# Kernel tuning notes

Measured on AMD Instinct MI355X. Metric: run time of the kernel, lower is better.

The kernel has to match this reference:

```python
import jax, jax.numpy as jnp
import numpy as np

B, N, FD = 2, 50000, 13
E = 250000
M, H = 128, 128          # message_dim, hidden_dim
EDGE_IN = 2 * FD + 8     # 34
NODE_IN = FD + 2 * M     # 269


def _mlp(x, w1, b1, w2, b2):
    return jnp.tanh(x @ w1 + b1) @ w2 + b2


def setup_inputs() -> dict:
    root = jax.random.key(0)
    k = lambda i: jax.random.fold_in(root, i)

    def lin(i, din, dout):
        w = jax.random.normal(k(i), (din, dout), jnp.float32) * np.float32(1.0 / np.sqrt(din))
        b = jax.random.normal(k(i + 100), (dout,), jnp.float32) * np.float32(0.01)
        return w, b

    ew1, eb1 = lin(1, EDGE_IN, H); ew2, eb2 = lin(2, H, M)      # mlp_edge
    ww1, wb1 = lin(3, EDGE_IN, H); ww2, wb2 = lin(4, H, 1)      # mlp_weight
    xw1, xb1 = lin(5, EDGE_IN, H); xw2, xb2 = lin(6, H, M)      # mlp_edge_world
    yw1, yb1 = lin(7, EDGE_IN, H); yw2, yb2 = lin(8, H, 1)      # mlp_weight_world
    nw1, nb1 = lin(9, NODE_IN, H); nw2, nb2 = lin(10, H, FD)    # mlp_node

    z_h = jax.random.normal(k(20), (B, N, FD), jnp.float32)
    edge_hh = jax.random.randint(k(21), (B, 2, E), 0, N, jnp.int32)
    edge_world = jax.random.randint(k(22), (B, 2, E), 0, N, jnp.int32)
    return dict(z_h=z_h, edge_hh=edge_hh, edge_world=edge_world,
                ew1=ew1, eb1=eb1, ew2=ew2, eb2=eb2,
                ww1=ww1, wb1=wb1, ww2=ww2, wb2=wb2,
                xw1=xw1, xb1=xb1, xw2=xw2, xb2=xb2,
                yw1=yw1, yb1=yb1, yw2=yw2, yb2=yb2,
                nw1=nw1, nb1=nb1, nw2=nw2, nb2=nb2)


def _edge_features(z, s, t):
    # z: (N, FD); s, t: (E,)
    pos, vel = z[:, 0:3], z[:, 3:6]
    diff = pos[s] - pos[t]                               # (E, 3)
    dist = jnp.sum(diff * diff, axis=-1, keepdims=True)  # (E, 1) squared distance
    vxc = jnp.cross(vel[s], vel[t])                      # (E, 3)
    vxn = jnp.linalg.norm(vxc, axis=-1, keepdims=True)   # (E, 1)
    return jnp.concatenate([diff, dist, vxc, vxn], axis=-1)  # (E, 8)


def reference(z_h, edge_hh, edge_world,
              ew1, eb1, ew2, eb2, ww1, wb1, ww2, wb2,
              xw1, xb1, xw2, xb2, yw1, yb1, yw2, yb2,
              nw1, nb1, nw2, nb2):
    n_nodes = z_h.shape[1]

    def per_batch(z, e_hh, e_w):
        # normal edges
        s, t = e_hh[0], e_hh[1]
        inp = jnp.concatenate([z[s], z[t], _edge_features(z, s, t)], axis=-1)  # (E, 34)
        m = _mlp(inp, ew1, eb1, ew2, eb2)                                       # (E, M)
        w = jax.nn.sigmoid(_mlp(inp, ww1, wb1, ww2, wb2))                       # (E, 1)
        agg_h = jnp.zeros((n_nodes, M), z.dtype).at[t].add(w * m)
        # world edges
        sw, tw = e_w[0], e_w[1]
        inpw = jnp.concatenate([z[sw], z[tw], _edge_features(z, sw, tw)], axis=-1)
        mw = _mlp(inpw, xw1, xb1, xw2, xb2)
        ww_ = jax.nn.sigmoid(_mlp(inpw, yw1, yb1, yw2, yb2))
        agg_w = jnp.zeros((n_nodes, M), z.dtype).at[tw].add(ww_ * mw)
        return agg_h, agg_w

    m_agg_h, m_agg_w = jax.vmap(per_batch)(z_h, edge_hh, edge_world)  # (B, N, M) each
    input_node = jnp.concatenate([z_h, m_agg_h, m_agg_w], axis=-1)    # (B, N, 269)
    delta_z_h = _mlp(input_node, nw1, nb1, nw2, nb2)                  # (B, N, 13)
    return delta_z_h
```

## Files before the change

### kernel.cpp

```cpp
#include <hip/hip_runtime.h>
#include <hip/hip_bf16.h>

#define B_   2
#define N_   50000
#define FD_  13
#define E_   250000
#define M_   128
#define H_   128

typedef __attribute__((ext_vector_type(8))) short  short8;
typedef __attribute__((ext_vector_type(8))) __bf16 bf16x8;
typedef __attribute__((ext_vector_type(4))) float  f32x4;
typedef __attribute__((ext_vector_type(4))) unsigned int uint4v;
typedef __attribute__((ext_vector_type(8))) unsigned short ushort8;

#define AGG_BYTES  (4ull * N_ * 128 * 4)
#define HIST_BYTES (4ull * N_ * 4)
#define SORT_BYTES (4ull * E_ * 4)
#define OFF_EW1 0u
#define OFF_WW1 8192u
#define OFF_EW2 16384u
#define OFF_XW1 32768u
#define OFF_YW1 40960u
#define OFF_XW2 49152u
#define OFF_NW1 65536u
#define OFF_NW2 102400u

__device__ __forceinline__ float bf2f(unsigned short u) {
    unsigned int v = ((unsigned int)u) << 16;
    return __builtin_bit_cast(float, v);
}
__device__ __forceinline__ unsigned short f2bf(float f) {
    __bf16 h = (__bf16)f;
    return __builtin_bit_cast(unsigned short, h);
}
__device__ __forceinline__ float tanh_fast(float x) {
    float e = __expf(x + x);
    float r = __builtin_amdgcn_rcpf(e + 1.0f);
    return __builtin_fmaf(-2.0f, r, 1.0f);
}
__device__ __forceinline__ float sigmoid_fast(float x) {
    return __builtin_amdgcn_rcpf(1.0f + __expf(-x));
}
__device__ __forceinline__ f32x4 mfma16(short8 a, short8 b, f32x4 c) {
    return __builtin_amdgcn_mfma_f32_16x16x32_bf16(
        __builtin_bit_cast(bf16x8, a), __builtin_bit_cast(bf16x8, b), c, 0, 0, 0);
}

__global__ void prep_kernel(const float* __restrict__ ew1, const float* __restrict__ ww1,
                            const float* __restrict__ ew2, const float* __restrict__ xw1,
                            const float* __restrict__ yw1, const float* __restrict__ xw2,
                            const float* __restrict__ nw1, const float* __restrict__ nw2,
                            unsigned short* __restrict__ fb, uint4v* __restrict__ hist4) {
    int m = blockIdx.y, f = blockIdx.x, l = threadIdx.x;
    {
        unsigned int flat = ((unsigned int)m * gridDim.x + (unsigned int)f) * 64u + (unsigned int)l;
        const uint4v zv = {0u, 0u, 0u, 0u};
        for (unsigned int i = flat; i < 50000u; i += gridDim.x * gridDim.y * 64u)
            hist4[i] = zv;
    }
    const float* src; int K, Nn, KS; unsigned int off;
    switch (m) {
        case 0: src = ew1; K = 34;  Nn = 128; KS = 2; off = OFF_EW1; break;
        case 1: src = ww1; K = 34;  Nn = 128; KS = 2; off = OFF_WW1; break;
        case 2: src = ew2; K = 128; Nn = 128; KS = 4; off = OFF_EW2; break;
        case 3: src = xw1; K = 34;  Nn = 128; KS = 2; off = OFF_XW1; break;
        case 4: src = yw1; K = 34;  Nn = 128; KS = 2; off = OFF_YW1; break;
        case 5: src = xw2; K = 128; Nn = 128; KS = 4; off = OFF_XW2; break;
        case 6: src = nw1; K = 269; Nn = 128; KS = 9; off = OFF_NW1; break;
        default: src = nw2; K = 128; Nn = 13; KS = 4; off = OFF_NW2; break;
    }
    int NT = (Nn + 15) / 16;
    if (f >= KS * NT) return;
    int ks = f / NT, nt = f % NT;
    int n = nt * 16 + (l & 15);
    unsigned short* dst = fb + off + ((unsigned int)f * 64u + (unsigned int)l) * 8u;
    #pragma unroll
    for (int j = 0; j < 8; j++) {
        int k = ks * 32 + ((l >> 4) * 8) + j;
        int kk = k; bool valid = (k < K) && (n < Nn);
        if (m == 6) {
            if (k < 256)      kk = k + 13;
            else if (k < 269) kk = k - 256;
            else              valid = false;
            valid = valid && (n < Nn);
        }
        dst[j] = valid ? f2bf(src[kk * Nn + n]) : (unsigned short)0;
    }
}

__global__ void hist_kernel(const int* __restrict__ ehh, const int* __restrict__ eww,
                            int* __restrict__ hist) {
    int p = blockIdx.y, idx = blockIdx.x * 256 + threadIdx.x;
    if (idx >= E_) return;
    const int* eg = ((p >> 1) ? eww : ehh) + (size_t)(p & 1) * 2 * E_;
    atomicAdd(&hist[p * N_ + eg[E_ + idx]], 1);
}

__global__ void scan_kernel(int* __restrict__ hist) {
    __shared__ int part[1024];
    const int p = blockIdx.x, tid = threadIdx.x;
    int* h = hist + p * N_;
    const int lo = tid * 52;
    int cnt = N_ - lo; if (cnt < 0) cnt = 0; if (cnt > 52) cnt = 52;
    int v[52];
    int sum = 0;
    if (cnt == 52) {
        const int4* src = (const int4*)(h + lo);
        #pragma unroll
        for (int i = 0; i < 13; i++) {
            int4 t = src[i];
            v[4*i] = t.x; v[4*i+1] = t.y; v[4*i+2] = t.z; v[4*i+3] = t.w;
        }
        #pragma unroll
        for (int i = 0; i < 52; i++) sum += v[i];
    } else {
        for (int i = 0; i < cnt; i++) sum += h[lo + i];
    }
    part[tid] = sum;
    __syncthreads();
    for (int off = 1; off < 1024; off <<= 1) {
        int t = (tid >= off) ? part[tid - off] : 0;
        __syncthreads();
        part[tid] += t;
        __syncthreads();
    }
    int excl = (tid == 0) ? 0 : part[tid - 1];
    if (cnt == 52) {
        int4* dst = (int4*)(h + lo);
        #pragma unroll
        for (int i = 0; i < 13; i++) {
            int4 o;
            o.x = excl; excl += v[4*i];
            o.y = excl; excl += v[4*i+1];
            o.z = excl; excl += v[4*i+2];
            o.w = excl; excl += v[4*i+3];
            dst[i] = o;
        }
    } else {
        for (int i = 0; i < cnt; i++) { int t = h[lo + i]; h[lo + i] = excl; excl += t; }
    }
}

__global__ void scatter_kernel(const int* __restrict__ ehh, const int* __restrict__ eww,
                               int* __restrict__ hist, unsigned int* __restrict__ sorted,
                               uint4v* __restrict__ agg4) {
    int p = blockIdx.y, idx = blockIdx.x * 256 + threadIdx.x;
    {
        unsigned int flat = ((unsigned int)p * gridDim.x + (unsigned int)blockIdx.x) * 256u
                          + (unsigned int)threadIdx.x;
        const unsigned int nthr = gridDim.x * gridDim.y * 256u;
        const uint4v zv = {0u, 0u, 0u, 0u};
        for (unsigned int i = flat; i < 6400000u; i += nthr) agg4[i] = zv;
    }
    if (idx >= E_) return;
    const int* eg = ((p >> 1) ? eww : ehh) + (size_t)(p & 1) * 2 * E_;
    int s = eg[idx];
    int t = eg[E_ + idx];
    int pos = atomicAdd(&hist[p * N_ + t], 1);
    sorted[(size_t)p * E_ + pos] = (unsigned int)s | ((unsigned int)t << 16);
}

__launch_bounds__(256, 3)
__global__ void edge_kernel_agg(const float* __restrict__ z,
                                const unsigned int* __restrict__ sorted,
                                const unsigned short* __restrict__ fb,
                                float* __restrict__ agg,
                                const float* __restrict__ eb1, const float* __restrict__ wb1,
                                const float* __restrict__ ww2, const float* __restrict__ wb2,
                                const float* __restrict__ eb2,
                                const float* __restrict__ xb1, const float* __restrict__ yb1,
                                const float* __restrict__ yw2, const float* __restrict__ yb2,
                                const float* __restrict__ xb2) {
    __shared__ alignas(16) unsigned short Abuf[128][48];
    __shared__ alignas(16) unsigned short Hbuf[128][136];
    __shared__ float w_acc[128];
    __shared__ int   tgt_s[128];

    const int tid  = threadIdx.x;
    const int lane = tid & 63, wv = tid >> 6, quad = lane >> 4, c = lane & 15;
    const int pass = blockIdx.y, b = pass & 1, set = pass >> 1;
    const int ebase = blockIdx.x * 128;

    const float* zb = z + (size_t)b * N_ * FD_;
    float* aggp = agg + (size_t)pass * N_ * 128;

    const short8* Fm1 = (const short8*)(fb + (set ? OFF_XW1 : OFF_EW1));
    const short8* Fw1 = (const short8*)(fb + (set ? OFF_YW1 : OFF_WW1));
    const short8* Fm2 = (const short8*)(fb + (set ? OFF_XW2 : OFF_EW2));
    const float* B1m = set ? xb1 : eb1;
    const float* B1w = set ? yb1 : wb1;
    const float* B2m = set ? xb2 : eb2;
    const float* Wv2 = set ? yw2 : ww2;
    const float wbias = (set ? yb2 : wb2)[0];

    const int nt0 = wv * 2;
    short8 bm[2][2], bw[2][2], b2f[2][4];
    float bias1m[2], bias1w[2], bias2m[2], w2v[2];
    #pragma unroll
    for (int i = 0; i < 2; i++) {
        int nt = nt0 + i, n = nt * 16 + c;
        #pragma unroll
        for (int ks = 0; ks < 2; ks++) { bm[i][ks] = Fm1[(ks * 8 + nt) * 64 + lane];
                                         bw[i][ks] = Fw1[(ks * 8 + nt) * 64 + lane]; }
        #pragma unroll
        for (int ks = 0; ks < 4; ks++) { b2f[i][ks] = Fm2[(ks * 8 + nt) * 64 + lane]; }
        bias1m[i] = B1m[n]; bias1w[i] = B1w[n];
        bias2m[i] = B2m[n]; w2v[i] = Wv2[n];
    }

    if (tid < 128) {
        const int e = tid;
        const int prt = e >> 4, pqd = (e >> 2) & 3, prr = e & 3;
        const int wpos = pqd * 32 + prt * 4 + prr;
        int sp = ebase + wpos;
        const bool valid = (sp < E_);
        if (!valid) sp = E_ - 1;
        unsigned int st = sorted[(size_t)pass * E_ + sp];
        int s = (int)(st & 0xffffu), t = (int)(st >> 16);
        tgt_s[e] = valid ? t : -1;
        w_acc[e] = 0.0f;
        const float* zs = zb + (size_t)s * 13;
        const float* zt = zb + (size_t)t * 13;
        float fs[13], ft[13];
        __builtin_memcpy(fs, zs, 13 * sizeof(float));
        __builtin_memcpy(ft, zt, 13 * sizeof(float));
        float d0 = fs[0] - ft[0], d1 = fs[1] - ft[1], d2 = fs[2] - ft[2];
        float dist = d0 * d0 + d1 * d1 + d2 * d2;
        float c0 = fs[4] * ft[5] - fs[5] * ft[4];
        float c1 = fs[5] * ft[3] - fs[3] * ft[5];
        float c2 = fs[3] * ft[4] - fs[4] * ft[3];
        float vxn = sqrtf(c0 * c0 + c1 * c1 + c2 * c2);
        unsigned short row[40];
        #pragma unroll
        for (int j = 0; j < 13; j++) { row[j] = f2bf(fs[j]); row[13 + j] = f2bf(ft[j]); }
        row[26] = f2bf(d0); row[27] = f2bf(d1); row[28] = f2bf(d2); row[29] = f2bf(dist);
        row[30] = f2bf(c0); row[31] = f2bf(c1); row[32] = f2bf(c2); row[33] = f2bf(vxn);
        #pragma unroll
        for (int j = 34; j < 40; j++) row[j] = 0;
        #pragma unroll
        for (int v = 0; v < 5; v++) {
            short8 sv;
            #pragma unroll
            for (int j = 0; j < 8; j++) sv[j] = (short)row[v * 8 + j];
            *((short8*)&Abuf[e][v * 8]) = sv;
        }
    }
    __syncthreads();

    #pragma unroll 1
    for (int rt = 0; rt < 8; rt++) {
        const unsigned short* ar = &Abuf[rt * 16 + c][0];
        short8 a0 = *((const short8*)(ar + quad * 8));
        short8 a1 = {};
        if (quad == 0) a1 = *((const short8*)(ar + 32));
        float wpart[4] = {0.f, 0.f, 0.f, 0.f};
        #pragma unroll
        for (int i = 0; i < 2; i++) {
            f32x4 accm = {bias1m[i], bias1m[i], bias1m[i], bias1m[i]};
            f32x4 accw = {bias1w[i], bias1w[i], bias1w[i], bias1w[i]};
            accm = mfma16(a0, bm[i][0], accm);
            accm = mfma16(a1, bm[i][1], accm);
            accw = mfma16(a0, bw[i][0], accw);
            accw = mfma16(a1, bw[i][1], accw);
            int n = (nt0 + i) * 16 + c;
            #pragma unroll
            for (int r = 0; r < 4; r++) {
                Hbuf[rt * 16 + quad * 4 + r][n] = f2bf(tanh_fast(accm[r]));
                wpart[r] += tanh_fast(accw[r]) * w2v[i];
            }
        }
        #pragma unroll
        for (int r = 0; r < 4; r++) {
            float v = wpart[r];
            v += __shfl_xor(v, 1); v += __shfl_xor(v, 2);
            v += __shfl_xor(v, 4); v += __shfl_xor(v, 8);
            if (c == r) atomicAdd(&w_acc[rt * 16 + quad * 4 + r], v);
        }
    }
    __syncthreads();
    if (tid < 128) w_acc[tid] = sigmoid_fast(w_acc[tid] + wbias);
    __syncthreads();

    {
        const int n0 = nt0 * 16 + c;
        const int n1 = n0 + 16;
        int   tp = -1;
        float va0 = 0.f, va1 = 0.f;
        bool  from_start = true;
        #pragma unroll 1
        for (int rt = 0; rt < 8; rt++) {
            const unsigned short* hr = &Hbuf[rt * 16 + c][0];
            short8 h0 = *((const short8*)(hr + quad * 8));
            short8 h1 = *((const short8*)(hr + 32 + quad * 8));
            short8 h2 = *((const short8*)(hr + 64 + quad * 8));
            short8 h3 = *((const short8*)(hr + 96 + quad * 8));
            f32x4 accA = {bias2m[0], bias2m[0], bias2m[0], bias2m[0]};
            f32x4 accB = {bias2m[1], bias2m[1], bias2m[1], bias2m[1]};
            accA = mfma16(h0, b2f[0][0], accA);
            accA = mfma16(h1, b2f[0][1], accA);
            accA = mfma16(h2, b2f[0][2], accA);
            accA = mfma16(h3, b2f[0][3], accA);
            accB = mfma16(h0, b2f[1][0], accB);
            accB = mfma16(h1, b2f[1][1], accB);
            accB = mfma16(h2, b2f[1][2], accB);
            accB = mfma16(h3, b2f[1][3], accB);
            const int elq = rt * 16 + quad * 4;
            #pragma unroll
            for (int r = 0; r < 4; r++) {
                const int row = elq + r;
                const int tg = tgt_s[row];
                const float g = w_acc[row];
                const float v0 = accA[r] * g;
                const float v1 = accB[r] * g;
                if (tg == tp) {
                    va0 += v0; va1 += v1;
                } else {
                    if (tp >= 0) {
                        float* dst = aggp + (size_t)tp * 128;
                        if (from_start) { atomicAdd(dst + n0, va0); atomicAdd(dst + n1, va1); }
                        else            { dst[n0] = va0; dst[n1] = va1; }
                    }
                    tp = tg; va0 = v0; va1 = v1;
                    from_start = (rt == 0 && r == 0);
                }
            }
        }
        if (tp >= 0) {
            float* dst = aggp + (size_t)tp * 128;
            atomicAdd(dst + n0, va0);
            atomicAdd(dst + n1, va1);
        }
    }
}

__launch_bounds__(256, 6)
__global__ void node_fused(const float* __restrict__ z,
                           const float* __restrict__ agg,
                           const unsigned short* __restrict__ fb,
                           const float* __restrict__ nb1,
                           const float* __restrict__ nb2,
                           float* __restrict__ out) {
    __shared__ alignas(16) unsigned short Abuf[16][296];
    __shared__ alignas(16) unsigned short Hbuf[16][136];

    const int tid  = threadIdx.x;
    const int lane = tid & 63, wv = tid >> 6, quad = lane >> 4, c = lane & 15;
    const int g0 = blockIdx.x * 16;

    {
        const int nl = tid >> 4;
        const int part = tid & 15;
        const int g = g0 + nl;
        const int b = (g >= N_) ? 1 : 0;
        const int t = g - b * N_;
        #pragma unroll
        for (int s = 0; s < 2; s++) {
            const float* ap = agg + ((size_t)(s * 2 + b) * N_ + t) * 128 + part * 8;
            f32x4 v0 = *(const f32x4*)(ap);
            f32x4 v1 = *(const f32x4*)(ap + 4);
            ushort8 u;
            #pragma unroll
            for (int k = 0; k < 4; k++) { u[k] = f2bf(v0[k]); u[4 + k] = f2bf(v1[k]); }
            *((ushort8*)&Abuf[nl][s * 128 + part * 8]) = u;
        }
    }
    for (int j = tid; j < 16 * 13; j += 256) {
        int nl = j / 13, k = j % 13;
        Abuf[nl][256 + k] = f2bf(z[(size_t)(g0 + nl) * 13 + k]);
    }
    for (int j = tid; j < 16 * 19; j += 256) {
        int nl = j / 19, k = j % 19;
        Abuf[nl][269 + k] = 0;
    }
    __syncthreads();

    {
        const short8* F1 = (const short8*)(fb + OFF_NW1);
        const int nt0 = wv * 2;
        const float b1a = nb1[nt0 * 16 + c];
        const float b1b = nb1[(nt0 + 1) * 16 + c];
        f32x4 acc0 = {b1a, b1a, b1a, b1a};
        f32x4 acc1 = {b1b, b1b, b1b, b1b};
        #pragma unroll
        for (int ks = 0; ks < 9; ks++) {
            short8 a = *((const short8*)(&Abuf[c][0] + ks * 32 + quad * 8));
            acc0 = mfma16(a, F1[(ks * 8 + nt0) * 64 + lane], acc0);
            acc1 = mfma16(a, F1[(ks * 8 + nt0 + 1) * 64 + lane], acc1);
        }
        #pragma unroll
        for (int r = 0; r < 4; r++) {
            Hbuf[quad * 4 + r][nt0 * 16 + c]       = f2bf(tanh_fast(acc0[r]));
            Hbuf[quad * 4 + r][(nt0 + 1) * 16 + c] = f2bf(tanh_fast(acc1[r]));
        }
    }
    __syncthreads();

    if (wv == 0) {
        const short8* F2 = (const short8*)(fb + OFF_NW2);
        const float bias2 = (c < 13) ? nb2[c] : 0.0f;
        f32x4 acc = {bias2, bias2, bias2, bias2};
        #pragma unroll
        for (int ks = 0; ks < 4; ks++) {
            short8 h = *((const short8*)(&Hbuf[c][0] + ks * 32 + quad * 8));
            acc = mfma16(h, F2[ks * 64 + lane], acc);
        }
        #pragma unroll
        for (int r = 0; r < 4; r++) {
            int g = g0 + quad * 4 + r;
            if (c < 13) out[(size_t)g * 13 + c] = acc[r];
        }
    }
}

extern "C" void kernel_launch(void* const* d_in, const int* in_sizes, int n_in,
                              void* d_out, int out_size, void* d_ws, size_t ws_size,
                              hipStream_t stream) {
    const float* z   = (const float*)d_in[0];
    const int* ehh   = (const int*)d_in[1];
    const int* eww   = (const int*)d_in[2];
    const float* ew1 = (const float*)d_in[3];
    const float* eb1 = (const float*)d_in[4];
    const float* ew2 = (const float*)d_in[5];
    const float* eb2 = (const float*)d_in[6];
    const float* ww1 = (const float*)d_in[7];
    const float* wb1 = (const float*)d_in[8];
    const float* ww2 = (const float*)d_in[9];
    const float* wb2 = (const float*)d_in[10];
    const float* xw1 = (const float*)d_in[11];
    const float* xb1 = (const float*)d_in[12];
    const float* xw2 = (const float*)d_in[13];
    const float* xb2 = (const float*)d_in[14];
    const float* yw1 = (const float*)d_in[15];
    const float* yb1 = (const float*)d_in[16];
    const float* yw2 = (const float*)d_in[17];
    const float* yb2 = (const float*)d_in[18];
    const float* nw1 = (const float*)d_in[19];
    const float* nb1 = (const float*)d_in[20];
    const float* nw2 = (const float*)d_in[21];
    const float* nb2 = (const float*)d_in[22];

    float* agg  = (float*)d_ws;
    int* hist   = (int*)((char*)d_ws + AGG_BYTES);
    unsigned int* sorted = (unsigned int*)((char*)d_ws + AGG_BYTES + HIST_BYTES);
    unsigned short* frag = (unsigned short*)((char*)d_ws + AGG_BYTES + HIST_BYTES + SORT_BYTES);

    prep_kernel<<<dim3(72, 8), 64, 0, stream>>>(ew1, ww1, ew2, xw1, yw1, xw2, nw1, nw2,
                                                frag, (uint4v*)hist);
    hist_kernel<<<dim3((E_ + 255) / 256, 4), 256, 0, stream>>>(ehh, eww, hist);
    scan_kernel<<<4, 1024, 0, stream>>>(hist);
    scatter_kernel<<<dim3((E_ + 255) / 256, 4), 256, 0, stream>>>(ehh, eww, hist, sorted,
                                                                  (uint4v*)agg);
    edge_kernel_agg<<<dim3((E_ + 127) / 128, 4), 256, 0, stream>>>(
        z, sorted, frag, agg,
        eb1, wb1, ww2, wb2, eb2,
        xb1, yb1, yw2, yb2, xb2);
    node_fused<<<(B_ * N_) / 16, 256, 0, stream>>>(
        z, agg, frag, nb1, nb2, (float*)d_out);
}
```

Before: 402.4 us.

## Make node MLP kernel persistent with register-prefetched double-buffered tiles

The node kernel now launches a fixed grid of 1024 blocks that loop over 16-node tiles instead of one block per tile. While the current tile is being computed, the aggregated message and z values for the next tile are loaded into registers, and the A buffer in shared memory is double-buffered so those loads overlap the MFMA work. Per-block setup such as biases, fragment pointers and padding zeroing is hoisted out of the loop. The cost is fewer resident blocks (launch bounds 6 to 4) and extra registers held for the prefetch, which could reduce how much memory latency the GPU hides.

```diff
diff --git a/kernel.cpp b/kernel.cpp
--- a/kernel.cpp
+++ b/kernel.cpp
@@ -334,82 +334,107 @@
     }
 }
 
-__launch_bounds__(256, 6)
+#define NODE_BLOCKS 1024
+__launch_bounds__(256, 4)
 __global__ void node_fused(const float* __restrict__ z,
                            const float* __restrict__ agg,
                            const unsigned short* __restrict__ fb,
                            const float* __restrict__ nb1,
                            const float* __restrict__ nb2,
                            float* __restrict__ out) {
-    __shared__ alignas(16) unsigned short Abuf[16][296];
+    __shared__ alignas(16) unsigned short Abuf[2][16][296];
     __shared__ alignas(16) unsigned short Hbuf[16][136];
 
     const int tid  = threadIdx.x;
     const int lane = tid & 63, wv = tid >> 6, quad = lane >> 4, c = lane & 15;
-    const int g0 = blockIdx.x * 16;
+    const int nl = tid >> 4, part = tid & 15;
+    constexpr int NT_TILES = (B_ * N_) / 16;
+
+    for (int j = tid; j < 2 * 16 * 19; j += 256) {
+        int bufi = j / (16 * 19), jj = j % (16 * 19);
+        Abuf[bufi][jj / 19][269 + jj % 19] = 0;
+    }
+
+    const short8* F1 = (const short8*)(fb + OFF_NW1);
+    const short8* F2 = (const short8*)(fb + OFF_NW2);
+    const int nt0 = wv * 2;
+    const float b1a = nb1[nt0 * 16 + c];
+    const float b1b = nb1[(nt0 + 1) * 16 + c];
+    const float bias2 = (c < 13) ? nb2[c] : 0.0f;
+
+    f32x4 pa0, pa1, pb0, pb1;
+    float pz = 0.0f;
+
+    int t = blockIdx.x;
 
     {
-        const int nl = tid >> 4;
-        const int part = tid & 15;
-        const int g = g0 + nl;
+        const int g = t * 16 + nl;
         const int b = (g >= N_) ? 1 : 0;
-        const int t = g - b * N_;
-        #pragma unroll
-        for (int s = 0; s < 2; s++) {
-            const float* ap = agg + ((size_t)(s * 2 + b) * N_ + t) * 128 + part * 8;
-            f32x4 v0 = *(const f32x4*)(ap);
-            f32x4 v1 = *(const f32x4*)(ap + 4);
+        const int tt = g - b * N_;
+        const float* ap0 = agg + ((size_t)b * N_ + tt) * 128 + part * 8;
+        const float* ap1 = agg + ((size_t)(2 + b) * N_ + tt) * 128 + part * 8;
+        pa0 = *(const f32x4*)(ap0); pa1 = *(const f32x4*)(ap0 + 4);
+        pb0 = *(const f32x4*)(ap1); pb1 = *(const f32x4*)(ap1 + 4);
+        if (tid < 208) pz = z[(size_t)(t * 16 + tid / 13) * 13 + (tid % 13)];
+    }
+
+    int buf = 0;
+    for (; t < NT_TILES; t += NODE_BLOCKS) {
+        const int g0 = t * 16;
+        {
             ushort8 u;
             #pragma unroll
-            for (int k = 0; k < 4; k++) { u[k] = f2bf(v0[k]); u[4 + k] = f2bf(v1[k]); }
-            *((ushort8*)&Abuf[nl][s * 128 + part * 8]) = u;
-        }
-    }
-    for (int j = tid; j < 16 * 13; j += 256) {
-        int nl = j / 13, k = j % 13;
-        Abuf[nl][256 + k] = f2bf(z[(size_t)(g0 + nl) * 13 + k]);
-    }
-    for (int j = tid; j < 16 * 19; j += 256) {
-        int nl = j / 19, k = j % 19;
-        Abuf[nl][269 + k] = 0;
-    }
-    __syncthreads();
-
-    {
-        const short8* F1 = (const short8*)(fb + OFF_NW1);
-        const int nt0 = wv * 2;
-        const float b1a = nb1[nt0 * 16 + c];
-        const float b1b = nb1[(nt0 + 1) * 16 + c];
-        f32x4 acc0 = {b1a, b1a, b1a, b1a};
-        f32x4 acc1 = {b1b, b1b, b1b, b1b};
-        #pragma unroll
-        for (int ks = 0; ks < 9; ks++) {
-            short8 a = *((const short8*)(&Abuf[c][0] + ks * 32 + quad * 8));
-            acc0 = mfma16(a, F1[(ks * 8 + nt0) * 64 + lane], acc0);
-            acc1 = mfma16(a, F1[(ks * 8 + nt0 + 1) * 64 + lane], acc1);
-        }
-        #pragma unroll
-        for (int r = 0; r < 4; r++) {
-            Hbuf[quad * 4 + r][nt0 * 16 + c]       = f2bf(tanh_fast(acc0[r]));
-            Hbuf[quad * 4 + r][(nt0 + 1) * 16 + c] = f2bf(tanh_fast(acc1[r]));
-        }
-    }
-    __syncthreads();
-
-    if (wv == 0) {
-        const short8* F2 = (const short8*)(fb + OFF_NW2);
-        const float bias2 = (c < 13) ? nb2[c] : 0.0f;
-        f32x4 acc = {bias2, bias2, bias2, bias2};
-        #pragma unroll
-        for (int ks = 0; ks < 4; ks++) {
-            short8 h = *((const short8*)(&Hbuf[c][0] + ks * 32 + quad * 8));
-            acc = mfma16(h, F2[ks * 64 + lane], acc);
-        }
-        #pragma unroll
-        for (int r = 0; r < 4; r++) {
-            int g = g0 + quad * 4 + r;
-            if (c < 13) out[(size_t)g * 13 + c] = acc[r];
-        }
+            for (int k = 0; k < 4; k++) { u[k] = f2bf(pa0[k]); u[4 + k] = f2bf(pa1[k]); }
+            *((ushort8*)&Abuf[buf][nl][part * 8]) = u;
+            #pragma unroll
+            for (int k = 0; k < 4; k++) { u[k] = f2bf(pb0[k]); u[4 + k] = f2bf(pb1[k]); }
+            *((ushort8*)&Abuf[buf][nl][128 + part * 8]) = u;
+            if (tid < 208) Abuf[buf][tid / 13][256 + tid % 13] = f2bf(pz);
+        }
+        const int tn = t + NODE_BLOCKS;
+        if (tn < NT_TILES) {
+            const int g = tn * 16 + nl;
+            const int b = (g >= N_) ? 1 : 0;
+            const int tt = g - b * N_;
+            const float* ap0 = agg + ((size_t)b * N_ + tt) * 128 + part * 8;
+            const float* ap1 = agg + ((size_t)(2 + b) * N_ + tt) * 128 + part * 8;
+            pa0 = *(const f32x4*)(ap0); pa1 = *(const f32x4*)(ap0 + 4);
+            pb0 = *(const f32x4*)(ap1); pb1 = *(const f32x4*)(ap1 + 4);
+            if (tid < 208) pz = z[(size_t)(tn * 16 + tid / 13) * 13 + (tid % 13)];
+        }
+        __syncthreads();
+
+        {
+            f32x4 acc0 = {b1a, b1a, b1a, b1a};
+            f32x4 acc1 = {b1b, b1b, b1b, b1b};
+            #pragma unroll
+            for (int ks = 0; ks < 9; ks++) {
+                short8 a = *((const short8*)(&Abuf[buf][c][0] + ks * 32 + quad * 8));
+                acc0 = mfma16(a, F1[(ks * 8 + nt0) * 64 + lane], acc0);
+                acc1 = mfma16(a, F1[(ks * 8 + nt0 + 1) * 64 + lane], acc1);
+            }
+            #pragma unroll
+            for (int r = 0; r < 4; r++) {
+                Hbuf[quad * 4 + r][nt0 * 16 + c]       = f2bf(tanh_fast(acc0[r]));
+                Hbuf[quad * 4 + r][(nt0 + 1) * 16 + c] = f2bf(tanh_fast(acc1[r]));
+            }
+        }
+        __syncthreads();
+
+        if (wv == 0) {
+            f32x4 acc = {bias2, bias2, bias2, bias2};
+            #pragma unroll
+            for (int ks = 0; ks < 4; ks++) {
+                short8 h = *((const short8*)(&Hbuf[c][0] + ks * 32 + quad * 8));
+                acc = mfma16(h, F2[ks * 64 + lane], acc);
+            }
+            #pragma unroll
+            for (int r = 0; r < 4; r++) {
+                int g = g0 + quad * 4 + r;
+                if (c < 13) out[(size_t)g * 13 + c] = acc[r];
+            }
+        }
+        buf ^= 1;
     }
 }
 
@@ -455,6 +480,6 @@
         z, sorted, frag, agg,
         eb1, wb1, ww2, wb2, eb2,
         xb1, yb1, yw2, yb2, xb2);
-    node_fused<<<(B_ * N_) / 16, 256, 0, stream>>>(
+    node_fused<<<NODE_BLOCKS, 256, 0, stream>>>(
         z, agg, frag, nb1, nb2, (float*)d_out);
 }
```

Measured after the change: 399.9 us. Within noise of the previous version (-0.6%).
